# Kernel tuning notes

Hardware: AMD Instinct MI355X
Metric: run time of the kernel (lower is better)

The kernel has to match this reference:

```python
import jax, jax.numpy as jnp
import numpy as np

GROUP_SIZE = 128
NIBBLES = 8  # int4 values packed per int32


def dequantize(qweight, qzeros, scales):
    """Unpack int4 weights/zeros and dequantize: w = (q - z) * scale.

    qweight: [in/8, out] int32, 8 int4 values packed along the IN dim.
    qzeros:  [groups, out/8] int32, 8 int4 zeros packed along the OUT dim.
    scales:  [groups, out] fp16.
    Returns w: [in, out] fp16.
    """
    shifts = (jnp.arange(NIBBLES, dtype=jnp.int32) * 4)
    # unpack weights along input dim -> [in/8, 8, out] -> [in, out]
    q = ((qweight[:, None, :] >> shifts[None, :, None]) & 15)
    q = q.reshape(-1, qweight.shape[1])
    # unpack zeros along output dim -> [groups, out/8, 8] -> [groups, out]
    z = ((qzeros[:, :, None] >> shifts[None, None, :]) & 15)
    z = z.reshape(qzeros.shape[0], -1)
    # broadcast per-group zeros/scales to per-input-row
    z_full = jnp.repeat(z, GROUP_SIZE, axis=0).astype(scales.dtype)   # [in, out]
    s_full = jnp.repeat(scales, GROUP_SIZE, axis=0)                    # [in, out]
    return (q.astype(scales.dtype) - z_full) * s_full


def setup_inputs() -> dict:
    key = jax.random.key(0)
    k1, k2, k3, k4, k5 = jax.random.split(key, 5)
    B, S, IN, OUT, G = 2, 2048, 4096, 11008, 32
    x = jax.random.normal(k1, (B, S, IN), dtype=jnp.float16)
    qweight = jax.random.randint(k2, (IN // 8, OUT), 0, 2147483647, dtype=jnp.int32)
    qzeros = jax.random.randint(k3, (G, OUT // 8), 0, 2147483647, dtype=jnp.int32)
    scales = jax.random.uniform(k4, (G, OUT), dtype=jnp.float16, minval=0.001, maxval=0.02)
    bias = jax.random.normal(k5, (OUT,), dtype=jnp.float16)
    return {"x": x, "qweight": qweight, "qzeros": qzeros, "scales": scales, "bias": bias}


def reference(x, qweight, qzeros, scales, bias):
    w = dequantize(qweight, qzeros, scales)  # [in, out] fp16
    # q4_matmul accumulates in fp32, emits fp16
    out = jnp.einsum('bsi,io->bso', x, w, preferred_element_type=jnp.float32)
    out = out.astype(jnp.float16) + bias
    return out
```

## Files before the change

kernel.cpp:

```cpp
#include <hip/hip_runtime.h>
#include <cstdint>
#include <cstddef>


typedef unsigned short u16;
typedef u16    u16x8  __attribute__((ext_vector_type(8)));
typedef __bf16 bfv8   __attribute__((ext_vector_type(8)));
typedef float  f32x4  __attribute__((ext_vector_type(4)));

#define K_DIM 4096
#define N_DIM 11008
#define GS    128
#define LSTR  72

__device__ __forceinline__ u16 f2bf(float f) {
  union { float f; uint32_t u; } v;
  v.f = f;
  uint32_t u = v.u + 0x7FFFu + ((v.u >> 16) & 1u);
  return (u16)(u >> 16);
}
__device__ __forceinline__ float f16r(float v) {
  return (float)(_Float16)v;
}

__global__ __launch_bounds__(256) void convert_x_kernel(
    const float* __restrict__ x, u16* __restrict__ xb) {
  const size_t i = ((size_t)blockIdx.x * 256 + threadIdx.x) * 8;
  const f32x4 a = *(const f32x4*)(x + i);
  const f32x4 b = *(const f32x4*)(x + i + 4);
  u16x8 o;
#pragma unroll
  for (int t = 0; t < 4; ++t) { o[t] = f2bf(a[t]); o[t + 4] = f2bf(b[t]); }
  *(u16x8*)(xb + i) = o;
}

__global__ __launch_bounds__(256) void dequant_kernel(
    const uint32_t* __restrict__ qweight, const uint32_t* __restrict__ qzeros,
    const float* __restrict__ scales, u16* __restrict__ wt) {
  const int kc = blockIdx.x;
  const int n  = blockIdx.y * 256 + threadIdx.x;
  const int g  = kc >> 1;

  const uint32_t zq = qzeros[(size_t)g * (N_DIM / 8) + (n >> 3)];
  const int   z   = (int)((zq >> ((n & 7) * 4)) & 15u);
  const float s   = scales[(size_t)g * N_DIM + n];
  const float nzs = -s * (float)z;

  u16* dst = wt + (size_t)n * K_DIM + kc * 64;
  const uint32_t* src = qweight + (size_t)(kc * 8) * N_DIM + n;
#pragma unroll
  for (int j = 0; j < 8; ++j) {
    const uint32_t q = src[(size_t)j * N_DIM];
    u16x8 w;
#pragma unroll
    for (int t = 0; t < 8; ++t) {
      const int qv = (int)((q >> (t * 4)) & 15u);
      w[t] = f2bf(fmaf((float)qv, s, nzs));
    }
    *(u16x8*)(dst + j * 8) = w;
  }
}

template <bool FUSED>
__global__ __launch_bounds__(256) void gemm_kernel(
    const u16* __restrict__ xb, const float* __restrict__ xf,
    const void* __restrict__ wsrc,
    const uint32_t* __restrict__ qzeros, const float* __restrict__ scales,
    const float* __restrict__ bias, float* __restrict__ out) {
  __shared__ __align__(16) u16 As[128 * LSTR];
  __shared__ __align__(16) u16 Bs[128 * LSTR];

  const int tid  = threadIdx.x;
  const int lane = tid & 63;
  const int wave = tid >> 6;
  const int n0 = blockIdx.x * 128;
  const int m0 = blockIdx.y * 128;

  const int m_off = (wave >> 1) * 64;
  const int n_off = (wave & 1) * 64;
  const int lrow  = lane & 15;
  const int lk    = lane >> 4;

  const int sm = tid >> 3;
  const int sc = tid & 7;

  const u16*      wt = (const u16*)wsrc;
  const uint32_t* qw = (const uint32_t*)wsrc;

  f32x4 acc[4][4];
#pragma unroll
  for (int i = 0; i < 4; ++i)
#pragma unroll
    for (int j = 0; j < 4; ++j) acc[i][j] = f32x4{0.f, 0.f, 0.f, 0.f};

  const int ncol = n0 + (tid & 127);
  float s_cur = 0.f, nzs_cur = 0.f;

  for (int kt = 0; kt < K_DIM / 64; ++kt) {
    const int k0 = kt * 64;

    u16x8 av[4];
    if (!FUSED) {
#pragma unroll
      for (int i = 0; i < 4; ++i) {
        const int m = i * 32 + sm;
        av[i] = *(const u16x8*)(xb + (size_t)(m0 + m) * K_DIM + (k0 + sc * 8));
      }
    } else {
#pragma unroll
      for (int i = 0; i < 4; ++i) {
        const int m = i * 32 + sm;
        const float* srcp = xf + (size_t)(m0 + m) * K_DIM + (k0 + sc * 8);
        const f32x4 p = *(const f32x4*)srcp;
        const f32x4 q4 = *(const f32x4*)(srcp + 4);
#pragma unroll
        for (int t = 0; t < 4; ++t) {
          av[i][t] = f2bf(p[t]);
          av[i][t + 4] = f2bf(q4[t]);
        }
      }
    }

    u16x8 bv[4];
    if (!FUSED) {
#pragma unroll
      for (int i = 0; i < 4; ++i) {
        const int n = i * 32 + sm;
        bv[i] = *(const u16x8*)(wt + (size_t)(n0 + n) * K_DIM + (k0 + sc * 8));
      }
    } else {
      if ((k0 & (GS - 1)) == 0) {
        const int g = k0 >> 7;
        const uint32_t zq = qzeros[(size_t)g * (N_DIM / 8) + (ncol >> 3)];
        const int z = (int)((zq >> ((ncol & 7) * 4)) & 15u);
        s_cur = scales[(size_t)g * N_DIM + ncol];
        nzs_cur = -s_cur * (float)z;
      }
#pragma unroll
      for (int i = 0; i < 4; ++i) {
        const int k8l = (tid >> 7) + i * 2;
        const uint32_t q = qw[(size_t)(k0 / 8 + k8l) * N_DIM + ncol];
#pragma unroll
        for (int t = 0; t < 8; ++t) {
          const int qv = (int)((q >> (t * 4)) & 15u);
          bv[i][t] = f2bf(fmaf((float)qv, s_cur, nzs_cur));
        }
      }
    }

#pragma unroll
    for (int i = 0; i < 4; ++i) {
      const int m = i * 32 + sm;
      *(u16x8*)&As[m * LSTR + sc * 8] = av[i];
    }
    if (!FUSED) {
#pragma unroll
      for (int i = 0; i < 4; ++i) {
        const int n = i * 32 + sm;
        *(u16x8*)&Bs[n * LSTR + sc * 8] = bv[i];
      }
    } else {
      const int nl = tid & 127;
#pragma unroll
      for (int i = 0; i < 4; ++i) {
        const int k8l = (tid >> 7) + i * 2;
        *(u16x8*)&Bs[nl * LSTR + k8l * 8] = bv[i];
      }
    }

    __syncthreads();

#pragma unroll
    for (int ks = 0; ks < 2; ++ks) {
      const int c = (ks * 4 + lk) * 8;
      bfv8 a[4], b[4];
#pragma unroll
      for (int i = 0; i < 4; ++i)
        a[i] = __builtin_bit_cast(bfv8,
                 *(const u16x8*)&As[(m_off + i * 16 + lrow) * LSTR + c]);
#pragma unroll
      for (int j = 0; j < 4; ++j)
        b[j] = __builtin_bit_cast(bfv8,
                 *(const u16x8*)&Bs[(n_off + j * 16 + lrow) * LSTR + c]);
#pragma unroll
      for (int i = 0; i < 4; ++i)
#pragma unroll
        for (int j = 0; j < 4; ++j)
          acc[i][j] = __builtin_amdgcn_mfma_f32_16x16x32_bf16(a[i], b[j],
                                                              acc[i][j], 0, 0, 0);
    }

    __syncthreads();
  }

#pragma unroll
  for (int j = 0; j < 4; ++j) {
    const int n = n0 + n_off + j * 16 + lrow;
    const float bvf = bias[n];
#pragma unroll
    for (int i = 0; i < 4; ++i) {
      const int mrow = m0 + m_off + i * 16 + lk * 4;
#pragma unroll
      for (int r = 0; r < 4; ++r) {
        out[(size_t)(mrow + r) * N_DIM + n] = f16r(f16r(acc[i][j][r]) + bvf);
      }
    }
  }
}

extern "C" void kernel_launch(void* const* d_in, const int* in_sizes, int n_in,
                              void* d_out, int out_size, void* d_ws, size_t ws_size,
                              hipStream_t stream) {
  const float* x = nullptr;      const uint32_t* qweight = nullptr;
  const uint32_t* qzeros = nullptr;
  const float* scales = nullptr; const float* bias = nullptr;
  int M = 4096;
  for (int i = 0; i < n_in; ++i) {
    const long long s = in_sizes[i];
    if      (s == (long long)(K_DIM / 8) * N_DIM) qweight = (const uint32_t*)d_in[i];
    else if (s == (long long)(K_DIM / GS) * (N_DIM / 8)) qzeros = (const uint32_t*)d_in[i];
    else if (s == (long long)(K_DIM / GS) * N_DIM) scales = (const float*)d_in[i];
    else if (s == (long long)N_DIM) bias = (const float*)d_in[i];
    else { x = (const float*)d_in[i]; M = (int)(s / K_DIM); }
  }
  float* out = (float*)d_out;

  const size_t xb_bytes = (size_t)M * K_DIM * sizeof(u16);
  const size_t wt_bytes = (size_t)N_DIM * K_DIM * sizeof(u16);

  if (ws_size >= xb_bytes + wt_bytes) {
    u16* xbp = (u16*)d_ws;
    u16* wtp = (u16*)((char*)d_ws + xb_bytes);
    convert_x_kernel<<<(int)((size_t)M * K_DIM / 2048), 256, 0, stream>>>(x, xbp);
    dequant_kernel<<<dim3(K_DIM / 64, N_DIM / 256), 256, 0, stream>>>(
        qweight, qzeros, scales, wtp);
    gemm_kernel<false><<<dim3(N_DIM / 128, M / 128), 256, 0, stream>>>(
        xbp, x, wtp, qzeros, scales, bias, out);
  } else {
    gemm_kernel<true><<<dim3(N_DIM / 128, M / 128), 256, 0, stream>>>(
        nullptr, x, qweight, qzeros, scales, bias, out);
  }
}
```

Before: 744.5 us.

## Pre-tile and swizzle operands so GEMM loads tiles via direct global-to-LDS copies

```diff
diff --git a/kernel.cpp b/kernel.cpp
--- a/kernel.cpp
+++ b/kernel.cpp
@@ -11,6 +11,7 @@
 #define K_DIM 4096
 #define N_DIM 11008
 #define GS    128
+#define KT    (K_DIM / 64)
 #define LSTR  72
 
 __device__ __forceinline__ u16 f2bf(float f) {
@@ -22,53 +23,65 @@
 __device__ __forceinline__ float f16r(float v) {
   return (float)(_Float16)v;
 }
-
-__global__ __launch_bounds__(256) void convert_x_kernel(
+__device__ __forceinline__ void async_load16(const u16* g, u16* l) {
+  __builtin_amdgcn_global_load_lds(
+      (const __attribute__((address_space(1))) uint32_t*)g,
+      (__attribute__((address_space(3))) uint32_t*)l, 16, 0, 0);
+}
+
+__global__ __launch_bounds__(256) void convert_x_tiled(
     const float* __restrict__ x, u16* __restrict__ xb) {
-  const size_t i = ((size_t)blockIdx.x * 256 + threadIdx.x) * 8;
-  const f32x4 a = *(const f32x4*)(x + i);
-  const f32x4 b = *(const f32x4*)(x + i + 4);
-  u16x8 o;
-#pragma unroll
-  for (int t = 0; t < 4; ++t) { o[t] = f2bf(a[t]); o[t + 4] = f2bf(b[t]); }
-  *(u16x8*)(xb + i) = o;
-}
-
-__global__ __launch_bounds__(256) void dequant_kernel(
+  const int kt = blockIdx.x, mt = blockIdx.y;
+  const int k0 = kt * 64, m0 = mt * 128;
+  u16* dst = xb + ((size_t)(mt * KT + kt)) * 8192;
+#pragma unroll
+  for (int i = 0; i < 4; ++i) {
+    const int g  = i * 256 + threadIdx.x;
+    const int nl = g >> 3;
+    const int cg = (g & 7) ^ (nl & 7);
+    const float* sp = x + (size_t)(m0 + nl) * K_DIM + (k0 + cg * 8);
+    const f32x4 p = *(const f32x4*)sp;
+    const f32x4 q = *(const f32x4*)(sp + 4);
+    u16x8 o;
+#pragma unroll
+    for (int t = 0; t < 4; ++t) { o[t] = f2bf(p[t]); o[t + 4] = f2bf(q[t]); }
+    *(u16x8*)(dst + (size_t)g * 8) = o;
+  }
+}
+
+__global__ __launch_bounds__(256) void dequant_tiled(
     const uint32_t* __restrict__ qweight, const uint32_t* __restrict__ qzeros,
     const float* __restrict__ scales, u16* __restrict__ wt) {
-  const int kc = blockIdx.x;
-  const int n  = blockIdx.y * 256 + threadIdx.x;
-  const int g  = kc >> 1;
-
-  const uint32_t zq = qzeros[(size_t)g * (N_DIM / 8) + (n >> 3)];
-  const int   z   = (int)((zq >> ((n & 7) * 4)) & 15u);
-  const float s   = scales[(size_t)g * N_DIM + n];
-  const float nzs = -s * (float)z;
-
-  u16* dst = wt + (size_t)n * K_DIM + kc * 64;
-  const uint32_t* src = qweight + (size_t)(kc * 8) * N_DIM + n;
-#pragma unroll
-  for (int j = 0; j < 8; ++j) {
-    const uint32_t q = src[(size_t)j * N_DIM];
-    u16x8 w;
+  const int kt = blockIdx.x, nt = blockIdx.y;
+  const int k0 = kt * 64, n0 = nt * 128;
+  const int gq = kt >> 1;
+  u16* dst = wt + ((size_t)(nt * KT + kt)) * 8192;
+#pragma unroll
+  for (int i = 0; i < 4; ++i) {
+    const int g  = i * 256 + threadIdx.x;
+    const int nl = g >> 3;
+    const int cg = (g & 7) ^ (nl & 7);
+    const int n  = n0 + nl;
+    const uint32_t zq = qzeros[(size_t)gq * (N_DIM / 8) + (n >> 3)];
+    const int   z   = (int)((zq >> ((n & 7) * 4)) & 15u);
+    const float s   = scales[(size_t)gq * N_DIM + n];
+    const float nzs = -s * (float)z;
+    const uint32_t q = qweight[(size_t)(k0 / 8 + cg) * N_DIM + n];
+    u16x8 o;
 #pragma unroll
     for (int t = 0; t < 8; ++t) {
       const int qv = (int)((q >> (t * 4)) & 15u);
-      w[t] = f2bf(fmaf((float)qv, s, nzs));
-    }
-    *(u16x8*)(dst + j * 8) = w;
-  }
-}
-
-template <bool FUSED>
-__global__ __launch_bounds__(256) void gemm_kernel(
-    const u16* __restrict__ xb, const float* __restrict__ xf,
-    const void* __restrict__ wsrc,
-    const uint32_t* __restrict__ qzeros, const float* __restrict__ scales,
+      o[t] = f2bf(fmaf((float)qv, s, nzs));
+    }
+    *(u16x8*)(dst + (size_t)g * 8) = o;
+  }
+}
+
+__global__ __launch_bounds__(256) void gemm_tiled(
+    const u16* __restrict__ xb, const u16* __restrict__ wt,
     const float* __restrict__ bias, float* __restrict__ out) {
-  __shared__ __align__(16) u16 As[128 * LSTR];
-  __shared__ __align__(16) u16 Bs[128 * LSTR];
+  __shared__ __align__(16) u16 As[8192];
+  __shared__ __align__(16) u16 Bs[8192];
 
   const int tid  = threadIdx.x;
   const int lane = tid & 63;
@@ -80,13 +93,88 @@
   const int n_off = (wave & 1) * 64;
   const int lrow  = lane & 15;
   const int lk    = lane >> 4;
-
+  const int sw    = lrow & 7;
+
+  const u16* abase = xb + (size_t)blockIdx.y * KT * 8192;
+  const u16* bbase = wt + (size_t)blockIdx.x * KT * 8192;
+
+  f32x4 acc[4][4];
+#pragma unroll
+  for (int i = 0; i < 4; ++i)
+#pragma unroll
+    for (int j = 0; j < 4; ++j) acc[i][j] = f32x4{0.f, 0.f, 0.f, 0.f};
+
+  for (int kt = 0; kt < KT; ++kt) {
+    const u16* ag = abase + (size_t)kt * 8192;
+    const u16* bg = bbase + (size_t)kt * 8192;
+#pragma unroll
+    for (int i = 0; i < 4; ++i) {
+      async_load16(ag + (size_t)(i * 256 + tid) * 8,
+                   As + (size_t)(i * 256 + wave * 64) * 8);
+      async_load16(bg + (size_t)(i * 256 + tid) * 8,
+                   Bs + (size_t)(i * 256 + wave * 64) * 8);
+    }
+    __syncthreads();
+
+#pragma unroll
+    for (int ks = 0; ks < 2; ++ks) {
+      const int kq = ks * 4 + lk;
+      const int c = (kq ^ sw) * 8;
+      bfv8 a[4], b[4];
+#pragma unroll
+      for (int i = 0; i < 4; ++i) {
+        const int mf = m_off + i * 16 + lrow;
+        a[i] = __builtin_bit_cast(bfv8, *(const u16x8*)&As[mf * 64 + c]);
+      }
+#pragma unroll
+      for (int j = 0; j < 4; ++j) {
+        const int nf = n_off + j * 16 + lrow;
+        b[j] = __builtin_bit_cast(bfv8, *(const u16x8*)&Bs[nf * 64 + c]);
+      }
+#pragma unroll
+      for (int i = 0; i < 4; ++i)
+#pragma unroll
+        for (int j = 0; j < 4; ++j)
+          acc[i][j] = __builtin_amdgcn_mfma_f32_16x16x32_bf16(a[i], b[j],
+                                                              acc[i][j], 0, 0, 0);
+    }
+    __syncthreads();
+  }
+
+#pragma unroll
+  for (int j = 0; j < 4; ++j) {
+    const int n = n0 + n_off + j * 16 + lrow;
+    const float bvf = bias[n];
+#pragma unroll
+    for (int i = 0; i < 4; ++i) {
+      const int mrow = m0 + m_off + i * 16 + lk * 4;
+#pragma unroll
+      for (int r = 0; r < 4; ++r) {
+        out[(size_t)(mrow + r) * N_DIM + n] = f16r(f16r(acc[i][j][r]) + bvf);
+      }
+    }
+  }
+}
+
+__global__ __launch_bounds__(256) void gemm_fused(
+    const float* __restrict__ xf, const uint32_t* __restrict__ qw,
+    const uint32_t* __restrict__ qzeros, const float* __restrict__ scales,
+    const float* __restrict__ bias, float* __restrict__ out) {
+  __shared__ __align__(16) u16 As[128 * LSTR];
+  __shared__ __align__(16) u16 Bs[128 * LSTR];
+
+  const int tid  = threadIdx.x;
+  const int lane = tid & 63;
+  const int wave = tid >> 6;
+  const int n0 = blockIdx.x * 128;
+  const int m0 = blockIdx.y * 128;
+  const int m_off = (wave >> 1) * 64;
+  const int n_off = (wave & 1) * 64;
+  const int lrow  = lane & 15;
+  const int lk    = lane >> 4;
   const int sm = tid >> 3;
   const int sc = tid & 7;
 
-  const u16*      wt = (const u16*)wsrc;
-  const uint32_t* qw = (const uint32_t*)wsrc;
-
   f32x4 acc[4][4];
 #pragma unroll
   for (int i = 0; i < 4; ++i)
@@ -96,70 +184,40 @@
   const int ncol = n0 + (tid & 127);
   float s_cur = 0.f, nzs_cur = 0.f;
 
-  for (int kt = 0; kt < K_DIM / 64; ++kt) {
+  for (int kt = 0; kt < KT; ++kt) {
     const int k0 = kt * 64;
-
     u16x8 av[4];
-    if (!FUSED) {
-#pragma unroll
-      for (int i = 0; i < 4; ++i) {
-        const int m = i * 32 + sm;
-        av[i] = *(const u16x8*)(xb + (size_t)(m0 + m) * K_DIM + (k0 + sc * 8));
-      }
-    } else {
-#pragma unroll
-      for (int i = 0; i < 4; ++i) {
-        const int m = i * 32 + sm;
-        const float* srcp = xf + (size_t)(m0 + m) * K_DIM + (k0 + sc * 8);
-        const f32x4 p = *(const f32x4*)srcp;
-        const f32x4 q4 = *(const f32x4*)(srcp + 4);
-#pragma unroll
-        for (int t = 0; t < 4; ++t) {
-          av[i][t] = f2bf(p[t]);
-          av[i][t + 4] = f2bf(q4[t]);
-        }
-      }
-    }
-
+#pragma unroll
+    for (int i = 0; i < 4; ++i) {
+      const int m = i * 32 + sm;
+      const float* sp = xf + (size_t)(m0 + m) * K_DIM + (k0 + sc * 8);
+      const f32x4 p = *(const f32x4*)sp;
+      const f32x4 q4 = *(const f32x4*)(sp + 4);
+#pragma unroll
+      for (int t = 0; t < 4; ++t) { av[i][t] = f2bf(p[t]); av[i][t+4] = f2bf(q4[t]); }
+    }
     u16x8 bv[4];
-    if (!FUSED) {
-#pragma unroll
-      for (int i = 0; i < 4; ++i) {
-        const int n = i * 32 + sm;
-        bv[i] = *(const u16x8*)(wt + (size_t)(n0 + n) * K_DIM + (k0 + sc * 8));
-      }
-    } else {
-      if ((k0 & (GS - 1)) == 0) {
-        const int g = k0 >> 7;
-        const uint32_t zq = qzeros[(size_t)g * (N_DIM / 8) + (ncol >> 3)];
-        const int z = (int)((zq >> ((ncol & 7) * 4)) & 15u);
-        s_cur = scales[(size_t)g * N_DIM + ncol];
-        nzs_cur = -s_cur * (float)z;
-      }
-#pragma unroll
-      for (int i = 0; i < 4; ++i) {
-        const int k8l = (tid >> 7) + i * 2;
-        const uint32_t q = qw[(size_t)(k0 / 8 + k8l) * N_DIM + ncol];
-#pragma unroll
-        for (int t = 0; t < 8; ++t) {
-          const int qv = (int)((q >> (t * 4)) & 15u);
-          bv[i][t] = f2bf(fmaf((float)qv, s_cur, nzs_cur));
-        }
-      }
-    }
-
-#pragma unroll
-    for (int i = 0; i < 4; ++i) {
-      const int m = i * 32 + sm;
-      *(u16x8*)&As[m * LSTR + sc * 8] = av[i];
-    }
-    if (!FUSED) {
-#pragma unroll
-      for (int i = 0; i < 4; ++i) {
-        const int n = i * 32 + sm;
-        *(u16x8*)&Bs[n * LSTR + sc * 8] = bv[i];
-      }
-    } else {
+    if ((k0 & (GS - 1)) == 0) {
+      const int g = k0 >> 7;
+      const uint32_t zq = qzeros[(size_t)g * (N_DIM / 8) + (ncol >> 3)];
+      const int z = (int)((zq >> ((ncol & 7) * 4)) & 15u);
+      s_cur = scales[(size_t)g * N_DIM + ncol];
+      nzs_cur = -s_cur * (float)z;
+    }
+#pragma unroll
+    for (int i = 0; i < 4; ++i) {
+      const int k8l = (tid >> 7) + i * 2;
+      const uint32_t q = qw[(size_t)(k0 / 8 + k8l) * N_DIM + ncol];
+#pragma unroll
+      for (int t = 0; t < 8; ++t) {
+        const int qv = (int)((q >> (t * 4)) & 15u);
+        bv[i][t] = f2bf(fmaf((float)qv, s_cur, nzs_cur));
+      }
+    }
+#pragma unroll
+    for (int i = 0; i < 4; ++i)
+      *(u16x8*)&As[(i * 32 + sm) * LSTR + sc * 8] = av[i];
+    {
       const int nl = tid & 127;
 #pragma unroll
       for (int i = 0; i < 4; ++i) {
@@ -167,9 +225,7 @@
         *(u16x8*)&Bs[nl * LSTR + k8l * 8] = bv[i];
       }
     }
-
-    __syncthreads();
-
+    __syncthreads();
 #pragma unroll
     for (int ks = 0; ks < 2; ++ks) {
       const int c = (ks * 4 + lk) * 8;
@@ -189,10 +245,8 @@
           acc[i][j] = __builtin_amdgcn_mfma_f32_16x16x32_bf16(a[i], b[j],
                                                               acc[i][j], 0, 0, 0);
     }
-
-    __syncthreads();
-  }
-
+    __syncthreads();
+  }
 #pragma unroll
   for (int j = 0; j < 4; ++j) {
     const int n = n0 + n_off + j * 16 + lrow;
@@ -201,9 +255,8 @@
     for (int i = 0; i < 4; ++i) {
       const int mrow = m0 + m_off + i * 16 + lk * 4;
 #pragma unroll
-      for (int r = 0; r < 4; ++r) {
+      for (int r = 0; r < 4; ++r)
         out[(size_t)(mrow + r) * N_DIM + n] = f16r(f16r(acc[i][j][r]) + bvf);
-      }
     }
   }
 }
@@ -231,13 +284,13 @@
   if (ws_size >= xb_bytes + wt_bytes) {
     u16* xbp = (u16*)d_ws;
     u16* wtp = (u16*)((char*)d_ws + xb_bytes);
-    convert_x_kernel<<<(int)((size_t)M * K_DIM / 2048), 256, 0, stream>>>(x, xbp);
-    dequant_kernel<<<dim3(K_DIM / 64, N_DIM / 256), 256, 0, stream>>>(
+    convert_x_tiled<<<dim3(KT, M / 128), 256, 0, stream>>>(x, xbp);
+    dequant_tiled<<<dim3(KT, N_DIM / 128), 256, 0, stream>>>(
         qweight, qzeros, scales, wtp);
-    gemm_kernel<false><<<dim3(N_DIM / 128, M / 128), 256, 0, stream>>>(
-        xbp, x, wtp, qzeros, scales, bias, out);
+    gemm_tiled<<<dim3(N_DIM / 128, M / 128), 256, 0, stream>>>(
+        xbp, wtp, bias, out);
   } else {
-    gemm_kernel<true><<<dim3(N_DIM / 128, M / 128), 256, 0, stream>>>(
-        nullptr, x, qweight, qzeros, scales, bias, out);
-  }
-}
+    gemm_fused<<<dim3(N_DIM / 128, M / 128), 256, 0, stream>>>(
+        x, qweight, qzeros, scales, bias, out);
+  }
+}
```

Result: no change. 740.0 us (-0.6%).
